# Optimization experiments

Hardware: AMD Instinct MI355X
Metric: run time of the kernel (lower is better)

Reference implementation:

```python
import jax, jax.numpy as jnp
import numpy as np

H = 12          # trees_num / n_heads
D_WEIGHT = 0.1  # opt['d_weight']
NEG = -1e9


def setup_inputs() -> dict:
    key = jax.random.key(0)
    ks = jax.random.split(key, 6)
    B, N, D = 8, 512, 768
    inp = {}
    inp["input"] = jax.random.normal(ks[0], (B, N, D), dtype=jnp.float32)
    inp["src_mask"] = jax.random.randint(ks[1], (B, 1, N), 0, 2).astype(jnp.int32)
    inp["dep_emb"] = jax.random.normal(ks[2], (B, N, N), dtype=jnp.float32)
    s = 1.0 / np.sqrt(D)
    inp["Wq"] = jax.random.normal(ks[3], (D, D), dtype=jnp.float32) * s
    inp["bq"] = jnp.zeros((D,), dtype=jnp.float32)
    inp["Wk"] = jax.random.normal(ks[4], (D, D), dtype=jnp.float32) * s
    inp["bk"] = jnp.zeros((D,), dtype=jnp.float32)
    return inp


def reference(input, src_mask, dep_emb, Wq, bq, Wk, bk):
    B, N, D = input.shape
    dk = D // H
    # Q/K projections -> [B, H, N, dk]
    q = (input @ Wq + bq).reshape(B, N, H, dk).transpose(0, 2, 1, 3)
    k = (input @ Wk + bk).reshape(B, N, H, dk).transpose(0, 2, 1, 3)
    # scaled scores [B, H, N, N]
    scores = jnp.einsum("bhqd,bhkd->bhqk", q, k) / jnp.sqrt(jnp.asarray(dk, input.dtype))
    # blend with dependency bias: dep_emb [B,N,N] -> [B,1,N,N]
    scores = (1.0 - D_WEIGHT) * scores + D_WEIGHT * dep_emb[:, None, :, :]
    # mask: src_mask [B,1,N] -> [B,1,1,N]; masked_fill(mask==0, -1e9)
    scores = jnp.where(src_mask[:, None, :, :] == 0, NEG, scores)
    p_attn = jax.nn.softmax(scores, axis=-1)  # [B, H, N, N]
    # original returns list of per-head [B,N,N]; full tensor is equivalent
    return p_attn
```

## Files before the change

kernel.cpp:

```cpp
#include <hip/hip_runtime.h>


typedef _Float16 f16;
typedef _Float16 f16x4 __attribute__((ext_vector_type(4)));
typedef _Float16 f16x8 __attribute__((ext_vector_type(8)));
typedef float    f32x4 __attribute__((ext_vector_type(4)));

#define NTOK   512
#define DMODEL 768
#define BATCH  8
#define NHEAD  12
#define NEGV   (-1e9f)
#define KPAD   72
#define DEPS   516
#define OUTS   68

__global__ __launch_bounds__(256)
void prep_kernel(const float* __restrict__ X, f16* __restrict__ Xh,
                 const float* __restrict__ Wq, const float* __restrict__ Wk,
                 f16* __restrict__ Wt) {
    const int bx = blockIdx.x;
    if (bx < 3072) {
        const size_t i = ((size_t)bx * 256 + threadIdx.x) * 4;
        float4 v = *(const float4*)&X[i];
        f16x4 h = { (f16)v.x, (f16)v.y, (f16)v.z, (f16)v.w };
        *(f16x4*)&Xh[i] = h;
    } else {
        __shared__ float tile[32][33];
        const int id = bx - 3072;
        const int kb = (id % 24) * 32;
        const int nb = (id / 24) * 32;
        const float* __restrict__ W = (nb < 768) ? Wq : Wk;
        const int nc = (nb < 768) ? nb : nb - 768;
        const int tx = threadIdx.x & 31, ty = threadIdx.x >> 5;
        #pragma unroll
        for (int i = 0; i < 4; ++i)
            tile[ty + i*8][tx] = W[(size_t)(kb + ty + i*8) * DMODEL + nc + tx];
        __syncthreads();
        #pragma unroll
        for (int i = 0; i < 4; ++i)
            Wt[(size_t)(nb + ty + i*8) * DMODEL + kb + tx] = (f16)tile[tx][ty + i*8];
    }
}

__global__ __launch_bounds__(256)
void proj_mfma(const f16* __restrict__ Xh, const f16* __restrict__ Wt,
               const float* __restrict__ bq, const float* __restrict__ bk,
               f16* __restrict__ QK) {
    const int m0 = blockIdx.x * 128;
    const int n0 = blockIdx.y * 128;
    const int tid = threadIdx.x;
    const int wid = tid >> 6, l = tid & 63;
    const int l15 = l & 15, quad = l >> 4;
    const int wm = (wid & 1) * 64;
    const int wn = (wid >> 1) * 64;

    __shared__ f16 As[128 * KPAD];
    __shared__ f16 Bs[128 * KPAD];

    f32x4 acc[4][4];
    #pragma unroll
    for (int i = 0; i < 4; ++i)
        #pragma unroll
        for (int j = 0; j < 4; ++j) acc[i][j] = (f32x4){0.f, 0.f, 0.f, 0.f};

    const int srow = tid >> 1;
    const int scol = (tid & 1) * 32;

    for (int kt = 0; kt < DMODEL; kt += 64) {
        const f16* __restrict__ Asrc = Xh + (size_t)(m0 + srow) * DMODEL + kt + scol;
        const f16* __restrict__ Bsrc = Wt + (size_t)(n0 + srow) * DMODEL + kt + scol;
        #pragma unroll
        for (int j = 0; j < 4; ++j) {
            f16x8 av = *(const f16x8*)(Asrc + j * 8);
            *(f16x8*)&As[srow * KPAD + scol + j * 8] = av;
        }
        #pragma unroll
        for (int j = 0; j < 4; ++j) {
            f16x8 bv = *(const f16x8*)(Bsrc + j * 8);
            *(f16x8*)&Bs[srow * KPAD + scol + j * 8] = bv;
        }
        __syncthreads();
        #pragma unroll
        for (int ks = 0; ks < 2; ++ks) {
            f16x8 a[4], b[4];
            #pragma unroll
            for (int mi = 0; mi < 4; ++mi)
                a[mi] = *(f16x8*)&As[(wm + mi*16 + l15) * KPAD + ks*32 + quad*8];
            #pragma unroll
            for (int ni = 0; ni < 4; ++ni)
                b[ni] = *(f16x8*)&Bs[(wn + ni*16 + l15) * KPAD + ks*32 + quad*8];
            #pragma unroll
            for (int mi = 0; mi < 4; ++mi)
                #pragma unroll
                for (int ni = 0; ni < 4; ++ni)
                    acc[mi][ni] = __builtin_amdgcn_mfma_f32_16x16x32_f16(
                        a[mi], b[ni], acc[mi][ni], 0, 0, 0);
        }
        __syncthreads();
    }

    const float SC = (1.0f - 0.1f) / 8.0f;
    #pragma unroll
    for (int ni = 0; ni < 4; ++ni) {
        const int col = n0 + wn + ni * 16 + l15;
        const bool isQ = (col < 768);
        const float bv = isQ ? bq[col] : bk[col - 768];
        const float sc = isQ ? SC : 1.0f;
        #pragma unroll
        for (int mi = 0; mi < 4; ++mi)
            #pragma unroll
            for (int r = 0; r < 4; ++r) {
                const int row = m0 + wm + mi * 16 + quad * 4 + r;
                QK[(size_t)row * 1536 + col] = (f16)((acc[mi][ni][r] + bv) * sc);
            }
    }
}

__global__ __launch_bounds__(384, 2)
void attn_mfma(const f16* __restrict__ QK, const float* __restrict__ dep,
               const int* __restrict__ mask, float* __restrict__ out) {
    const int qt = blockIdx.x;
    const int hg = blockIdx.y;
    const int b  = blockIdx.z;
    const int tid = threadIdx.x;
    const int wid = tid >> 6;
    const int l   = tid & 63;
    const int l15 = l & 15, quad = l >> 4;
    const int h  = hg * 6 + wid;
    const int q0 = qt * 16;

    __shared__ float depL[16 * DEPS];
    __shared__ float outL[6 * 16 * OUTS];

    {
        const float* __restrict__ src = dep + ((size_t)b * NTOK + q0) * NTOK;
        #pragma unroll
        for (int i = 0; i < 6; ++i) {
            const int idx = tid + i * 384;
            if (idx < 2048) {
                const int row = idx >> 7, c4 = idx & 127;
                float4 v = *(const float4*)&src[(size_t)row * NTOK + c4 * 4];
                *(float4*)&depL[row * DEPS + c4 * 4] = v;
            }
        }
    }
    __syncthreads();

    f32x4 acc[32];
    #pragma unroll
    for (int t = 0; t < 32; ++t) acc[t] = (f32x4){0.f, 0.f, 0.f, 0.f};

    const f16* __restrict__ Qb = QK + (size_t)(b * NTOK + q0 + l15) * 1536 + h * 64 + quad * 8;
    const f16x8 qf0 = *(const f16x8*)(Qb);
    const f16x8 qf1 = *(const f16x8*)(Qb + 32);

    const f16* __restrict__ Kb = QK + (size_t)(b * NTOK + l15) * 1536 + 768 + h * 64 + quad * 8;
    #pragma unroll
    for (int t = 0; t < 32; ++t) {
        f16x8 k0 = *(const f16x8*)(Kb + (size_t)(t * 16) * 1536);
        acc[t] = __builtin_amdgcn_mfma_f32_16x16x32_f16(qf0, k0, acc[t], 0, 0, 0);
        f16x8 k1 = *(const f16x8*)(Kb + (size_t)(t * 16) * 1536 + 32);
        acc[t] = __builtin_amdgcn_mfma_f32_16x16x32_f16(qf1, k1, acc[t], 0, 0, 0);
    }

    const float DW = 0.1f;
    const int* __restrict__ mrow = mask + b * NTOK;
    #pragma unroll
    for (int t = 0; t < 32; ++t) {
        const int col = t * 16 + l15;
        const int mv = mrow[col];
        #pragma unroll
        for (int r = 0; r < 4; ++r) {
            const float dv = depL[(quad * 4 + r) * DEPS + col];
            const float s = acc[t][r] + DW * dv;
            acc[t][r] = mv ? s : NEGV;
        }
    }

    float rmax[4] = {NEGV, NEGV, NEGV, NEGV};
    #pragma unroll
    for (int t = 0; t < 32; ++t)
        #pragma unroll
        for (int r = 0; r < 4; ++r) rmax[r] = fmaxf(rmax[r], acc[t][r]);
    #pragma unroll
    for (int r = 0; r < 4; ++r) {
        rmax[r] = fmaxf(rmax[r], __shfl_xor(rmax[r], 1));
        rmax[r] = fmaxf(rmax[r], __shfl_xor(rmax[r], 2));
        rmax[r] = fmaxf(rmax[r], __shfl_xor(rmax[r], 4));
        rmax[r] = fmaxf(rmax[r], __shfl_xor(rmax[r], 8));
    }
    float rsum[4] = {0.f, 0.f, 0.f, 0.f};
    #pragma unroll
    for (int t = 0; t < 32; ++t)
        #pragma unroll
        for (int r = 0; r < 4; ++r) {
            const float e = __expf(acc[t][r] - rmax[r]);
            acc[t][r] = e;
            rsum[r] += e;
        }
    #pragma unroll
    for (int r = 0; r < 4; ++r) {
        rsum[r] += __shfl_xor(rsum[r], 1);
        rsum[r] += __shfl_xor(rsum[r], 2);
        rsum[r] += __shfl_xor(rsum[r], 4);
        rsum[r] += __shfl_xor(rsum[r], 8);
    }
    float inv[4];
    #pragma unroll
    for (int r = 0; r < 4; ++r) inv[r] = 1.0f / rsum[r];

    float* __restrict__ wOut = &outL[wid * 16 * OUTS];
    const size_t obase = ((size_t)((b * NHEAD + h) * NTOK) + q0) * NTOK;
    #pragma unroll
    for (int c = 0; c < 8; ++c) {
        #pragma unroll
        for (int tc = 0; tc < 4; ++tc) {
            const int t = c * 4 + tc;
            #pragma unroll
            for (int r = 0; r < 4; ++r)
                wOut[(quad * 4 + r) * OUTS + tc * 16 + l15] = acc[t][r] * inv[r];
        }
        #pragma unroll
        for (int j = 0; j < 4; ++j) {
            const int row = j * 4 + quad;
            const int c4  = l15;
            float4 v = *(float4*)&wOut[row * OUTS + c4 * 4];
            *(float4*)&out[obase + (size_t)row * NTOK + c * 64 + c4 * 4] = v;
        }
    }
}

extern "C" void kernel_launch(void* const* d_in, const int* in_sizes, int n_in,
                              void* d_out, int out_size, void* d_ws, size_t ws_size,
                              hipStream_t stream) {
    const float* X    = (const float*)d_in[0];
    const int*   mask = (const int*)  d_in[1];
    const float* dep  = (const float*)d_in[2];
    const float* Wq   = (const float*)d_in[3];
    const float* bq   = (const float*)d_in[4];
    const float* Wk   = (const float*)d_in[5];
    const float* bk   = (const float*)d_in[6];
    float* out = (float*)d_out;

    f16* Xh = (f16*)d_ws;
    f16* Wt = Xh + (size_t)BATCH * NTOK * DMODEL;
    f16* QK = Wt + (size_t)1536 * DMODEL;

    prep_kernel<<<dim3(3072 + 1152), 256, 0, stream>>>(X, Xh, Wq, Wk, Wt);
    proj_mfma<<<dim3(4096 / 128, 1536 / 128), 256, 0, stream>>>(Xh, Wt, bq, bk, QK);
    attn_mfma<<<dim3(32, 2, BATCH), 384, 0, stream>>>(QK, dep, mask, out);
}
```

Before: 186.4 us.

## Split attention rows across wave pairs and premultiply dep bias with mask in LDS

Each head's 512 key columns are now split across two waves, each holding 16 accumulators instead of 32. The pair combines row max and row sum through small shared-memory reductions with block barriers. The grid doubles to 4 head groups of 3 heads. The dependency tile is stored pre-scaled by 0.1 and with masked positions set to -2e9, which removes the per-element mask load and select. The output staging buffer reuses the depL shared memory, so less LDS and fewer registers are used and occupancy should rise. The cost is extra barriers and reloading the dep tile for twice as many blocks.

```diff
diff --git a/kernel.cpp b/kernel.cpp
--- a/kernel.cpp
+++ b/kernel.cpp
@@ -10,7 +10,6 @@
 #define DMODEL 768
 #define BATCH  8
 #define NHEAD  12
-#define NEGV   (-1e9f)
 #define KPAD   72
 #define DEPS   516
 #define OUTS   68
@@ -117,7 +116,7 @@
     }
 }
 
-__global__ __launch_bounds__(384, 2)
+__global__ __launch_bounds__(384)
 void attn_mfma(const f16* __restrict__ QK, const float* __restrict__ dep,
                const int* __restrict__ mask, float* __restrict__ out) {
     const int qt = blockIdx.x;
@@ -127,60 +126,63 @@
     const int wid = tid >> 6;
     const int l   = tid & 63;
     const int l15 = l & 15, quad = l >> 4;
-    const int h  = hg * 6 + wid;
-    const int q0 = qt * 16;
+    const int hl  = wid >> 1;
+    const int ch  = wid & 1;
+    const int h   = hg * 3 + hl;
+    const int q0  = qt * 16;
 
     __shared__ float depL[16 * DEPS];
-    __shared__ float outL[6 * 16 * OUTS];
+    __shared__ float redmax[3][16][2];
+    __shared__ float redsum[3][16][2];
 
     {
         const float* __restrict__ src = dep + ((size_t)b * NTOK + q0) * NTOK;
+        const int*   __restrict__ msk = mask + b * NTOK;
         #pragma unroll
         for (int i = 0; i < 6; ++i) {
             const int idx = tid + i * 384;
             if (idx < 2048) {
                 const int row = idx >> 7, c4 = idx & 127;
-                float4 v = *(const float4*)&src[(size_t)row * NTOK + c4 * 4];
-                *(float4*)&depL[row * DEPS + c4 * 4] = v;
+                float4 dv = *(const float4*)&src[(size_t)row * NTOK + c4 * 4];
+                int4   mv = *(const int4*)  &msk[c4 * 4];
+                float4 o = { mv.x ? 0.1f * dv.x : -2e9f,
+                             mv.y ? 0.1f * dv.y : -2e9f,
+                             mv.z ? 0.1f * dv.z : -2e9f,
+                             mv.w ? 0.1f * dv.w : -2e9f };
+                *(float4*)&depL[row * DEPS + c4 * 4] = o;
             }
         }
     }
     __syncthreads();
 
-    f32x4 acc[32];
-    #pragma unroll
-    for (int t = 0; t < 32; ++t) acc[t] = (f32x4){0.f, 0.f, 0.f, 0.f};
+    f32x4 acc[16];
+    #pragma unroll
+    for (int t = 0; t < 16; ++t) acc[t] = (f32x4){0.f, 0.f, 0.f, 0.f};
 
     const f16* __restrict__ Qb = QK + (size_t)(b * NTOK + q0 + l15) * 1536 + h * 64 + quad * 8;
     const f16x8 qf0 = *(const f16x8*)(Qb);
     const f16x8 qf1 = *(const f16x8*)(Qb + 32);
 
-    const f16* __restrict__ Kb = QK + (size_t)(b * NTOK + l15) * 1536 + 768 + h * 64 + quad * 8;
-    #pragma unroll
-    for (int t = 0; t < 32; ++t) {
+    const f16* __restrict__ Kb = QK + (size_t)(b * NTOK + ch * 256 + l15) * 1536 + 768 + h * 64 + quad * 8;
+    #pragma unroll
+    for (int t = 0; t < 16; ++t) {
         f16x8 k0 = *(const f16x8*)(Kb + (size_t)(t * 16) * 1536);
         acc[t] = __builtin_amdgcn_mfma_f32_16x16x32_f16(qf0, k0, acc[t], 0, 0, 0);
         f16x8 k1 = *(const f16x8*)(Kb + (size_t)(t * 16) * 1536 + 32);
         acc[t] = __builtin_amdgcn_mfma_f32_16x16x32_f16(qf1, k1, acc[t], 0, 0, 0);
     }
 
-    const float DW = 0.1f;
-    const int* __restrict__ mrow = mask + b * NTOK;
-    #pragma unroll
-    for (int t = 0; t < 32; ++t) {
-        const int col = t * 16 + l15;
-        const int mv = mrow[col];
-        #pragma unroll
-        for (int r = 0; r < 4; ++r) {
-            const float dv = depL[(quad * 4 + r) * DEPS + col];
-            const float s = acc[t][r] + DW * dv;
-            acc[t][r] = mv ? s : NEGV;
-        }
-    }
-
-    float rmax[4] = {NEGV, NEGV, NEGV, NEGV};
-    #pragma unroll
-    for (int t = 0; t < 32; ++t)
+    #pragma unroll
+    for (int t = 0; t < 16; ++t) {
+        const int col = ch * 256 + t * 16 + l15;
+        #pragma unroll
+        for (int r = 0; r < 4; ++r)
+            acc[t][r] += depL[(quad * 4 + r) * DEPS + col];
+    }
+
+    float rmax[4] = {-3e9f, -3e9f, -3e9f, -3e9f};
+    #pragma unroll
+    for (int t = 0; t < 16; ++t)
         #pragma unroll
         for (int r = 0; r < 4; ++r) rmax[r] = fmaxf(rmax[r], acc[t][r]);
     #pragma unroll
@@ -190,9 +192,18 @@
         rmax[r] = fmaxf(rmax[r], __shfl_xor(rmax[r], 4));
         rmax[r] = fmaxf(rmax[r], __shfl_xor(rmax[r], 8));
     }
+    if (l15 == 0) {
+        #pragma unroll
+        for (int r = 0; r < 4; ++r) redmax[hl][quad * 4 + r][ch] = rmax[r];
+    }
+    __syncthreads();
+    #pragma unroll
+    for (int r = 0; r < 4; ++r)
+        rmax[r] = fmaxf(rmax[r], redmax[hl][quad * 4 + r][ch ^ 1]);
+
     float rsum[4] = {0.f, 0.f, 0.f, 0.f};
     #pragma unroll
-    for (int t = 0; t < 32; ++t)
+    for (int t = 0; t < 16; ++t)
         #pragma unroll
         for (int r = 0; r < 4; ++r) {
             const float e = __expf(acc[t][r] - rmax[r]);
@@ -206,14 +217,20 @@
         rsum[r] += __shfl_xor(rsum[r], 4);
         rsum[r] += __shfl_xor(rsum[r], 8);
     }
+    if (l15 == 0) {
+        #pragma unroll
+        for (int r = 0; r < 4; ++r) redsum[hl][quad * 4 + r][ch] = rsum[r];
+    }
+    __syncthreads();
     float inv[4];
     #pragma unroll
-    for (int r = 0; r < 4; ++r) inv[r] = 1.0f / rsum[r];
-
-    float* __restrict__ wOut = &outL[wid * 16 * OUTS];
-    const size_t obase = ((size_t)((b * NHEAD + h) * NTOK) + q0) * NTOK;
-    #pragma unroll
-    for (int c = 0; c < 8; ++c) {
+    for (int r = 0; r < 4; ++r)
+        inv[r] = 1.0f / (rsum[r] + redsum[hl][quad * 4 + r][ch ^ 1]);
+
+    float* __restrict__ wOut = &depL[wid * 16 * OUTS];
+    const size_t obase = ((size_t)((b * NHEAD + h) * NTOK) + q0) * NTOK + ch * 256;
+    #pragma unroll
+    for (int c = 0; c < 4; ++c) {
         #pragma unroll
         for (int tc = 0; tc < 4; ++tc) {
             const int t = c * 4 + tc;
@@ -224,9 +241,8 @@
         #pragma unroll
         for (int j = 0; j < 4; ++j) {
             const int row = j * 4 + quad;
-            const int c4  = l15;
-            float4 v = *(float4*)&wOut[row * OUTS + c4 * 4];
-            *(float4*)&out[obase + (size_t)row * NTOK + c * 64 + c4 * 4] = v;
+            float4 v = *(float4*)&wOut[row * OUTS + l15 * 4];
+            *(float4*)&out[obase + (size_t)row * NTOK + c * 64 + l15 * 4] = v;
         }
     }
 }
@@ -249,5 +265,5 @@
 
     prep_kernel<<<dim3(3072 + 1152), 256, 0, stream>>>(X, Xh, Wq, Wk, Wt);
     proj_mfma<<<dim3(4096 / 128, 1536 / 128), 256, 0, stream>>>(Xh, Wt, bq, bk, QK);
-    attn_mfma<<<dim3(32, 2, BATCH), 384, 0, stream>>>(QK, dep, mask, out);
-}
+    attn_mfma<<<dim3(32, 4, BATCH), 384, 0, stream>>>(QK, dep, mask, out);
+}
```

New measurement: 196.4 us. 1.05x slower.
